# Performance work log

Measured on AMD Instinct MI355X. Metric: run time of the kernel, lower is better.

## Reference

```python
import jax, jax.numpy as jnp
import numpy as np

BETA_MIN, BETA_MAX = 0.01, 0.995
EPS_DELTA, EPS_RMS = 1e-6, 1e-5


def _rmsnorm(x, w):
    ms = jnp.mean(x * x, axis=-1, keepdims=True)
    return x * jax.lax.rsqrt(ms + EPS_RMS) * w


def _delta_scan(q, k, v, beta, mask, bb1, bb2):
    # q, k, v: [B, S, D]; beta, mask: [B, S, 1]; bb1, bb2: scalars
    phi_q = jax.nn.elu(q) + 1.0
    phi_k = jax.nn.elu(k) + 1.0
    b1_base = jnp.clip(jax.nn.sigmoid(bb1), BETA_MIN, BETA_MAX)
    b2_base = jnp.clip(jax.nn.sigmoid(bb2), BETA_MIN, BETA_MAX)
    B, S, D = q.shape

    def step(carry, inp):
        H1, H2, Z1, Z2 = carry
        qt, kt, vt, bt, mt = inp  # qt/kt/vt: [B,D], bt/mt: [B,1]
        bin_t = jnp.clip(bt, BETA_MIN, BETA_MAX)
        b1 = jnp.clip(b1_base * bin_t, BETA_MIN, BETA_MAX)  # [B,1]
        b2 = jnp.clip(b2_base * bin_t, BETA_MIN, BETA_MAX)
        kv = jnp.einsum('bd,be->bde', kt, vt) * mt[:, :, None]  # [B,D,D]
        H1 = H1 * b1[:, :, None] + kv
        H2 = H2 * b2[:, :, None] + kv
        km = kt * mt
        Z1 = Z1 * b1 + km
        Z2 = Z2 * b2 + km
        num = jnp.einsum('bd,bde->be', qt, H1 + H2)
        den = jnp.maximum(jnp.sum(qt * (Z1 + Z2), axis=-1, keepdims=True), EPS_DELTA)
        return (H1, H2, Z1, Z2), num / den * mt

    init = (jnp.zeros((B, D, D), q.dtype), jnp.zeros((B, D, D), q.dtype),
            jnp.zeros((B, D), q.dtype), jnp.zeros((B, D), q.dtype))
    xs = tuple(a.swapaxes(0, 1) for a in (phi_q, phi_k, v, beta, mask))
    _, outs = jax.lax.scan(step, init, xs)
    return outs.swapaxes(0, 1)  # [B, S, D]


def setup_inputs() -> dict:
    key = jax.random.key(0)
    B, S, Dm, H = 4, 2048, 512, 8
    ks = jax.random.split(key, 8)
    scale = float(1.0 / np.sqrt(Dm))
    return {
        'x': jax.random.normal(ks[0], (B, S, Dm), jnp.float32),
        'mask': jnp.ones((B, S), jnp.float32),
        'Wq': jax.random.normal(ks[1], (Dm, Dm), jnp.float32) * scale,
        'Wk': jax.random.normal(ks[2], (Dm, Dm), jnp.float32) * scale,
        'Wv': jax.random.normal(ks[3], (Dm, Dm), jnp.float32) * scale,
        'Wb': jax.random.normal(ks[4], (H, Dm), jnp.float32) * scale,
        'bb': jnp.full((H,), 1.5, jnp.float32),
        'Wo': jax.random.normal(ks[5], (Dm, Dm), jnp.float32) * scale,
        'bo': jnp.zeros((Dm,), jnp.float32),
        'ln_w': jnp.ones((Dm,), jnp.float32),
        'recency': jnp.zeros((H,), jnp.float32),
        'base_beta_1': jnp.asarray(2.0, jnp.float32),
        'base_beta_2': jnp.asarray(3.0, jnp.float32),
    }


def reference(x, mask, Wq, Wk, Wv, Wb, bb, Wo, bo, ln_w, recency,
              base_beta_1, base_beta_2):
    B, S, Dm = x.shape
    H = recency.shape[0]
    d = Dm // H
    h = _rmsnorm(x, ln_w)
    q = h @ Wq.T
    k = h @ Wk.T
    v = h @ Wv.T
    # input-conditioned gate with per-head recency bias  -> [B, S, H]
    beta = jax.nn.sigmoid(h @ Wb.T + bb + recency)

    def to_heads(t):  # [B,S,Dm] -> [B*H, S, d]
        return t.reshape(B, S, H, d).transpose(0, 2, 1, 3).reshape(B * H, S, d)

    qh, kh, vh = to_heads(q), to_heads(k), to_heads(v)
    betah = beta.transpose(0, 2, 1).reshape(B * H, S, 1)
    maskh = jnp.broadcast_to(mask[:, None, :, None], (B, H, S, 1)).reshape(B * H, S, 1)
    o = _delta_scan(qh, kh, vh, betah, maskh, base_beta_1, base_beta_2)
    o = o.reshape(B, H, S, d).transpose(0, 2, 1, 3).reshape(B, S, Dm)
    return x + (o @ Wo.T + bo)
```

## Files before the change

### kernel.cpp

```cpp
#include <hip/hip_runtime.h>
#include <stdint.h>

typedef unsigned short u16;
typedef short bf16x8 __attribute__((ext_vector_type(8)));
typedef unsigned short u16x8 __attribute__((ext_vector_type(8)));
typedef unsigned short u16x4 __attribute__((ext_vector_type(4)));
typedef float f32x4 __attribute__((ext_vector_type(4)));

#define S_ 2048
#define DM 512
#define DH 64
#define CL 64
#define NCH 32

#define SW(r, sc) ((r) * 72 + ((sc) ^ (((r) & 7) << 3)))

__device__ __forceinline__ float b2f(u16 u) { return __uint_as_float(((unsigned)u) << 16); }
__device__ __forceinline__ u16 f2b(float f) {
    unsigned v = __float_as_uint(f);
    unsigned r = v + 0x7fffu + ((v >> 16) & 1u);
    return (u16)(r >> 16);
}
__device__ __forceinline__ float phi_elu(float x) { return x > 0.f ? x + 1.f : __expf(x); }
__device__ __forceinline__ float clip01(float v) { return fminf(fmaxf(v, 0.01f), 0.995f); }

__device__ __forceinline__ void gload16(const u16* g, u16* l) {
    __builtin_amdgcn_global_load_lds((const __attribute__((address_space(1))) void*)g,
                                     (__attribute__((address_space(3))) void*)l, 16, 0, 0);
}

__global__ __launch_bounds__(256) void k_rb(const float* __restrict__ x, const float* __restrict__ lnw,
                                            const float* __restrict__ Wb, const float* __restrict__ bb,
                                            const float* __restrict__ rec, const float* __restrict__ bb1p,
                                            const float* __restrict__ bb2p, u16* __restrict__ h,
                                            float* __restrict__ lb1, float* __restrict__ lb2) {
    int wave = threadIdx.x >> 6, lane = threadIdx.x & 63;
    int row = blockIdx.x * 4 + wave;
    const float* xr = x + (size_t)row * DM + lane * 8;
    float4 v0 = *(const float4*)xr;
    float4 v1 = *(const float4*)(xr + 4);
    float ss = v0.x * v0.x + v0.y * v0.y + v0.z * v0.z + v0.w * v0.w +
               v1.x * v1.x + v1.y * v1.y + v1.z * v1.z + v1.w * v1.w;
    #pragma unroll
    for (int off = 32; off; off >>= 1) ss += __shfl_xor(ss, off, 64);
    float sc = rsqrtf(ss * (1.f / DM) + 1e-5f);
    const float* wr_ = lnw + lane * 8;
    float4 w0 = *(const float4*)wr_;
    float4 w1 = *(const float4*)(wr_ + 4);
    float hv[8];
    hv[0] = v0.x * sc * w0.x; hv[1] = v0.y * sc * w0.y;
    hv[2] = v0.z * sc * w0.z; hv[3] = v0.w * sc * w0.w;
    hv[4] = v1.x * sc * w1.x; hv[5] = v1.y * sc * w1.y;
    hv[6] = v1.z * sc * w1.z; hv[7] = v1.w * sc * w1.w;
    u16x8 o;
    #pragma unroll
    for (int j = 0; j < 8; j++) o[j] = f2b(hv[j]);
    *(u16x8*)(h + (size_t)row * DM + lane * 8) = o;
    float acc[8];
    #pragma unroll
    for (int hd = 0; hd < 8; hd++) {
        const float* wp = Wb + hd * DM + lane * 8;
        float4 a0 = *(const float4*)wp;
        float4 a1 = *(const float4*)(wp + 4);
        acc[hd] = hv[0] * a0.x + hv[1] * a0.y + hv[2] * a0.z + hv[3] * a0.w +
                  hv[4] * a1.x + hv[5] * a1.y + hv[6] * a1.z + hv[7] * a1.w;
    }
    #pragma unroll
    for (int hd = 0; hd < 8; hd++) {
        #pragma unroll
        for (int off = 32; off; off >>= 1) acc[hd] += __shfl_xor(acc[hd], off, 64);
    }
    if (lane == 0) {
        float b1b = clip01(1.f / (1.f + __expf(-bb1p[0])));
        float b2b = clip01(1.f / (1.f + __expf(-bb2p[0])));
        int b = row >> 11, s = row & 2047;
        #pragma unroll
        for (int hd = 0; hd < 8; hd++) {
            float logit = acc[hd] + bb[hd] + rec[hd];
            float beta = 1.f / (1.f + __expf(-logit));
            float bin = clip01(beta);
            float b1 = clip01(b1b * bin);
            float b2 = clip01(b2b * bin);
            size_t o2 = (size_t)((b << 3) + hd) * S_ + s;
            lb1[o2] = log2f(b1);
            lb2[o2] = log2f(b2);
        }
    }
}

__global__ __launch_bounds__(256) void k_convw(const float* __restrict__ Wq, const float* __restrict__ Wk,
                                               const float* __restrict__ Wv, const float* __restrict__ Wo,
                                               u16* __restrict__ wcat, u16* __restrict__ wo) {
    int idx = blockIdx.x * 256 + threadIdx.x;
    int e0 = idx << 2;
    if (e0 < 1536 * 512) {
        int r = e0 >> 9, ccol = e0 & 511;
        const float* src = (r < 512) ? (Wq + (size_t)r * 512)
                         : (r < 1024) ? (Wk + (size_t)(r - 512) * 512)
                                      : (Wv + (size_t)(r - 1024) * 512);
        float4 v = *(const float4*)(src + ccol);
        u16x4 o = {f2b(v.x), f2b(v.y), f2b(v.z), f2b(v.w)};
        *(u16x4*)(wcat + e0) = o;
    } else {
        int e = e0 - 1536 * 512;
        float4 v = *(const float4*)(Wo + e);
        u16x4 o = {f2b(v.x), f2b(v.y), f2b(v.z), f2b(v.w)};
        *(u16x4*)(wo + e) = o;
    }
}

template<int MODE>
__global__ __launch_bounds__(256) void k_gemm(const u16* __restrict__ A, const u16* __restrict__ Bw, int K,
                                              const float* __restrict__ mask, u16* __restrict__ qh,
                                              u16* __restrict__ kh, u16* __restrict__ vh,
                                              const float* __restrict__ xres, const float* __restrict__ bo,
                                              float* __restrict__ outp) {
    __shared__ u16 As[128 * 32];
    __shared__ u16 Bs[128 * 32];
    int tid = threadIdx.x;
    int lane = tid & 63, w = tid >> 6;
    int wr = w >> 1, wc = w & 1;
    int m0 = blockIdx.x * 128, n0 = blockIdx.y * 128;
    f32x4 acc[4][4] = {};
    int srow = w * 32 + (lane >> 2);
    int skel = (lane & 3) << 3;
    const u16* gA0 = A + (size_t)(m0 + srow) * K + skel;
    const u16* gA1 = gA0 + (size_t)16 * K;
    const u16* gB0 = Bw + (size_t)(n0 + srow) * K + skel;
    const u16* gB1 = gB0 + (size_t)16 * K;
    u16* lA0 = &As[(w * 32) * 32];
    u16* lA1 = &As[(w * 32 + 16) * 32];
    u16* lB0 = &Bs[(w * 32) * 32];
    u16* lB1 = &Bs[(w * 32 + 16) * 32];
    int l15 = lane & 15, kh8 = (lane >> 4) << 3;
    for (int k0 = 0; k0 < K; k0 += 32) {
        if (k0) __syncthreads();
        gload16(gA0 + k0, lA0);
        gload16(gA1 + k0, lA1);
        gload16(gB0 + k0, lB0);
        gload16(gB1 + k0, lB1);
        __syncthreads();
        bf16x8 af[4], bfr[4];
        #pragma unroll
        for (int m = 0; m < 4; m++) af[m] = *(const bf16x8*)&As[(wr * 64 + m * 16 + l15) * 32 + kh8];
        #pragma unroll
        for (int n = 0; n < 4; n++) bfr[n] = *(const bf16x8*)&Bs[(wc * 64 + n * 16 + l15) * 32 + kh8];
        #pragma unroll
        for (int m = 0; m < 4; m++)
            #pragma unroll
            for (int n = 0; n < 4; n++)
                acc[m][n] = __builtin_amdgcn_mfma_f32_16x16x32_bf16(af[m], bfr[n], acc[m][n], 0, 0, 0);
    }
    #pragma unroll
    for (int m = 0; m < 4; m++) {
        int rbase = m0 + wr * 64 + m * 16 + ((lane >> 4) << 2);
        #pragma unroll
        for (int n = 0; n < 4; n++) {
            int col = n0 + wc * 64 + n * 16 + l15;
            #pragma unroll
            for (int r = 0; r < 4; r++) {
                int row = rbase + r;
                float v = acc[m][n][r];
                if constexpr (MODE == 0) {
                    int mat = col >> 9, f = col & 511, hh = f >> 6, j = f & 63;
                    int b = row >> 11, s = row & 2047;
                    size_t di = ((size_t)((b << 3) + hh) * S_ + s) * DH + j;
                    if (mat == 0) qh[di] = f2b(phi_elu(v));
                    else if (mat == 1) kh[di] = f2b(phi_elu(v) * mask[(b << 11) + s]);
                    else vh[di] = f2b(v);
                } else {
                    size_t oi = (size_t)row * DM + col;
                    outp[oi] = v + xres[oi] + bo[col];
                }
            }
        }
    }
}

__global__ __launch_bounds__(256) void k_pass1(const u16* __restrict__ kh, const u16* __restrict__ vh,
                                               const float* __restrict__ lb1, const float* __restrict__ lb2,
                                               u16* __restrict__ S1b, u16* __restrict__ S2b,
                                               float* __restrict__ z1, float* __restrict__ z2,
                                               float* __restrict__ P1, float* __restrict__ P2) {
    __shared__ u16 Kw1[64 * 72];
    __shared__ u16 Kw2[64 * 72];
    __shared__ u16 Vt[64 * 72];
    __shared__ float Ls1[64], Ls2[64];
    int tid = threadIdx.x;
    int bh = blockIdx.x >> 5, c = blockIdx.x & 31;
    int wave = tid >> 6, lane = tid & 63;
    size_t base = ((size_t)bh * S_ + c * CL) * DH;
    if (wave == 0) {
        float v = lb1[(size_t)bh * S_ + c * CL + lane];
        #pragma unroll
        for (int d = 1; d < 64; d <<= 1) { float o = __shfl_up(v, d, 64); if (lane >= d) v += o; }
        Ls1[lane] = v;
    } else if (wave == 1) {
        float v = lb2[(size_t)bh * S_ + c * CL + lane];
        #pragma unroll
        for (int d = 1; d < 64; d <<= 1) { float o = __shfl_up(v, d, 64); if (lane >= d) v += o; }
        Ls2[lane] = v;
    }
    int ss = tid & 63, i0 = (tid >> 6) << 4;
    const u16* kr = kh + base + (size_t)ss * DH + i0;
    u16x8 kk0 = *(const u16x8*)kr;
    u16x8 kk1 = *(const u16x8*)(kr + 8);
    {
        const u16* vr = vh + base + (size_t)ss * DH + i0;
        u16x8 vv0 = *(const u16x8*)vr;
        u16x8 vv1 = *(const u16x8*)(vr + 8);
        #pragma unroll
        for (int j = 0; j < 8; j++) {
            Vt[SW(i0 + j, ss)] = vv0[j];
            Vt[SW(i0 + 8 + j, ss)] = vv1[j];
        }
    }
    __syncthreads();
    float w1 = exp2f(Ls1[63] - Ls1[ss]);
    float w2 = exp2f(Ls2[63] - Ls2[ss]);
    #pragma unroll
    for (int j = 0; j < 8; j++) {
        float k0 = b2f(kk0[j]), k1 = b2f(kk1[j]);
        Kw1[SW(i0 + j, ss)] = f2b(w1 * k0);
        Kw2[SW(i0 + j, ss)] = f2b(w2 * k0);
        Kw1[SW(i0 + 8 + j, ss)] = f2b(w1 * k1);
        Kw2[SW(i0 + 8 + j, ss)] = f2b(w2 * k1);
    }
    if (tid == 0) { P1[blockIdx.x] = exp2f(Ls1[63]); P2[blockIdx.x] = exp2f(Ls2[63]); }
    __syncthreads();
    int l15 = lane & 15, kh8 = (lane >> 4) << 3;
    int j0 = wave << 4;
    bf16x8 vf0 = *(const bf16x8*)&Vt[SW(j0 + l15, kh8)];
    bf16x8 vf1 = *(const bf16x8*)&Vt[SW(j0 + l15, 32 + kh8)];
    f32x4 a1[4], a2[4];
    #pragma unroll
    for (int it = 0; it < 4; it++) { a1[it] = (f32x4){0,0,0,0}; a2[it] = (f32x4){0,0,0,0}; }
    #pragma unroll
    for (int it = 0; it < 4; it++) {
        int ir = (it << 4) + l15;
        bf16x8 b0 = *(const bf16x8*)&Kw1[SW(ir, kh8)];
        bf16x8 b1 = *(const bf16x8*)&Kw1[SW(ir, 32 + kh8)];
        a1[it] = __builtin_amdgcn_mfma_f32_16x16x32_bf16(vf0, b0, a1[it], 0, 0, 0);
        a1[it] = __builtin_amdgcn_mfma_f32_16x16x32_bf16(vf1, b1, a1[it], 0, 0, 0);
        bf16x8 c0 = *(const bf16x8*)&Kw2[SW(ir, kh8)];
        bf16x8 c1 = *(const bf16x8*)&Kw2[SW(ir, 32 + kh8)];
        a2[it] = __builtin_amdgcn_mfma_f32_16x16x32_bf16(vf0, c0, a2[it], 0, 0, 0);
        a2[it] = __builtin_amdgcn_mfma_f32_16x16x32_bf16(vf1, c1, a2[it], 0, 0, 0);
    }
    {
        int iz = tid >> 2, sg = tid & 3;
        u16x8 x0 = *(const u16x8*)&Kw1[SW(iz, sg << 4)];
        u16x8 x1 = *(const u16x8*)&Kw1[SW(iz, (sg << 4) + 8)];
        u16x8 y0 = *(const u16x8*)&Kw2[SW(iz, sg << 4)];
        u16x8 y1 = *(const u16x8*)&Kw2[SW(iz, (sg << 4) + 8)];
        float z1v = 0.f, z2v = 0.f;
        #pragma unroll
        for (int j = 0; j < 8; j++) {
            z1v += b2f(x0[j]) + b2f(x1[j]);
            z2v += b2f(y0[j]) + b2f(y1[j]);
        }
        z1v += __shfl_xor(z1v, 1, 64); z1v += __shfl_xor(z1v, 2, 64);
        z2v += __shfl_xor(z2v, 1, 64); z2v += __shfl_xor(z2v, 2, 64);
        if (sg == 0) {
            z1[(size_t)blockIdx.x * 64 + iz] = z1v;
            z2[(size_t)blockIdx.x * 64 + iz] = z2v;
        }
    }
    int jr0 = j0 + ((lane >> 4) << 2);
    size_t so = (size_t)blockIdx.x * 4096;
    #pragma unroll
    for (int it = 0; it < 4; it++) {
        int ii = (it << 4) + l15;
        #pragma unroll
        for (int r = 0; r < 4; r++) {
            S1b[so + (size_t)(jr0 + r) * 64 + ii] = f2b(a1[it][r]);
            S2b[so + (size_t)(jr0 + r) * 64 + ii] = f2b(a2[it][r]);
        }
    }
}

__global__ __launch_bounds__(256) void k_pass2(u16* __restrict__ S1b, u16* __restrict__ S2b,
                                               float* __restrict__ z1, float* __restrict__ z2,
                                               const float* __restrict__ P1, const float* __restrict__ P2) {
    int bh = blockIdx.x >> 1, part = blockIdx.x & 1;
    int e0 = (part * 256 + threadIdx.x) * 8;
    float c1[8] = {}, c2[8] = {};
    for (int c = 0; c < NCH; c++) {
        int bc = bh * NCH + c;
        size_t idx = (size_t)bc * 4096 + e0;
        u16x8 s1 = *(const u16x8*)&S1b[idx];
        u16x8 s2 = *(const u16x8*)&S2b[idx];
        float p1 = P1[bc], p2 = P2[bc];
        u16x8 o1, o2;
        #pragma unroll
        for (int j = 0; j < 8; j++) {
            o1[j] = f2b(c1[j]); c1[j] = c1[j] * p1 + b2f(s1[j]);
            o2[j] = f2b(c2[j]); c2[j] = c2[j] * p2 + b2f(s2[j]);
        }
        *(u16x8*)&S1b[idx] = o1;
        *(u16x8*)&S2b[idx] = o2;
    }
    if (part == 0 && threadIdx.x < 64) {
        float y1 = 0.f, y2 = 0.f;
        for (int c = 0; c < NCH; c++) {
            int bc = bh * NCH + c;
            size_t zi = (size_t)bc * 64 + threadIdx.x;
            float p1 = P1[bc], p2 = P2[bc];
            float t1 = z1[zi]; z1[zi] = y1; y1 = y1 * p1 + t1;
            float t2 = z2[zi]; z2[zi] = y2; y2 = y2 * p2 + t2;
        }
    }
}

__global__ __launch_bounds__(256) void k_pass3(const u16* __restrict__ qh, const u16* __restrict__ kh,
                                               const u16* __restrict__ vh, const float* __restrict__ lb1,
                                               const float* __restrict__ lb2, const u16* __restrict__ S1b,
                                               const u16* __restrict__ S2b, const float* __restrict__ z1,
                                               const float* __restrict__ z2, const float* __restrict__ mask,
                                               u16* __restrict__ obf) {
    __shared__ u16 Vt[64 * 72];
    __shared__ u16 AWs[64 * 72];
    __shared__ float Ls1[64], Ls2[64], dens[64], qZ1[64], qZ2[64];
    int tid = threadIdx.x;
    int bh = blockIdx.x >> 5, c = blockIdx.x & 31;
    int wave = tid >> 6, lane = tid & 63;
    size_t base = ((size_t)bh * S_ + c * CL) * DH;
    if (wave == 0) {
        float v = lb1[(size_t)bh * S_ + c * CL + lane];
        #pragma unroll
        for (int d = 1; d < 64; d <<= 1) { float o = __shfl_up(v, d, 64); if (lane >= d) v += o; }
        Ls1[lane] = v;
    } else if (wave == 1) {
        float v = lb2[(size_t)bh * S_ + c * CL + lane];
        #pragma unroll
        for (int d = 1; d < 64; d <<= 1) { float o = __shfl_up(v, d, 64); if (lane >= d) v += o; }
        Ls2[lane] = v;
    }
    {
        int ss = tid & 63, i0 = (tid >> 6) << 4;
        const u16* vr = vh + base + (size_t)ss * DH + i0;
        u16x8 vv0 = *(const u16x8*)vr;
        u16x8 vv1 = *(const u16x8*)(vr + 8);
        #pragma unroll
        for (int j = 0; j < 8; j++) {
            Vt[SW(i0 + j, ss)] = vv0[j];
            Vt[SW(i0 + 8 + j, ss)] = vv1[j];
        }
    }
    {
        int t = tid >> 2, g = tid & 3;
        const u16* qp = qh + base + (size_t)t * DH + (g << 4);
        u16x8 q0 = *(const u16x8*)qp;
        u16x8 q1 = *(const u16x8*)(qp + 8);
        const float* z1p = z1 + (size_t)blockIdx.x * 64 + (g << 4);
        const float* z2p = z2 + (size_t)blockIdx.x * 64 + (g << 4);
        float az1 = 0.f, az2 = 0.f;
        #pragma unroll
        for (int m = 0; m < 8; m++) {
            float qv0 = b2f(q0[m]), qv1 = b2f(q1[m]);
            az1 += qv0 * z1p[m] + qv1 * z1p[m + 8];
            az2 += qv0 * z2p[m] + qv1 * z2p[m + 8];
        }
        az1 += __shfl_xor(az1, 1, 64); az1 += __shfl_xor(az1, 2, 64);
        az2 += __shfl_xor(az2, 1, 64); az2 += __shfl_xor(az2, 2, 64);
        if (g == 0) { qZ1[t] = az1; qZ2[t] = az2; }
    }
    int l15 = lane & 15, kh8 = (lane >> 4) << 3;
    int t0 = wave << 4;
    const u16* qb = qh + base + (size_t)(t0 + l15) * DH;
    bf16x8 qf0 = *(const bf16x8*)(qb + kh8);
    bf16x8 qf1 = *(const bf16x8*)(qb + 32 + kh8);
    f32x4 accA[4];
    #pragma unroll
    for (int st = 0; st < 4; st++) accA[st] = (f32x4){0, 0, 0, 0};
    #pragma unroll
    for (int st = 0; st < 4; st++) {
        const u16* kb = kh + base + (size_t)((st << 4) + l15) * DH;
        bf16x8 kf0 = *(const bf16x8*)(kb + kh8);
        bf16x8 kf1 = *(const bf16x8*)(kb + 32 + kh8);
        accA[st] = __builtin_amdgcn_mfma_f32_16x16x32_bf16(qf0, kf0, accA[st], 0, 0, 0);
        accA[st] = __builtin_amdgcn_mfma_f32_16x16x32_bf16(qf1, kf1, accA[st], 0, 0, 0);
    }
    __syncthreads();
    int trow = t0 + ((lane >> 4) << 2);
    float l1t[4], l2t[4];
    #pragma unroll
    for (int r = 0; r < 4; r++) { l1t[r] = Ls1[trow + r]; l2t[r] = Ls2[trow + r]; }
    float rs[4] = {0.f, 0.f, 0.f, 0.f};
    #pragma unroll
    for (int st = 0; st < 4; st++) {
        int s = (st << 4) + l15;
        float s1 = Ls1[s], s2 = Ls2[s];
        #pragma unroll
        for (int r = 0; r < 4; r++) {
            float w = 0.f;
            if (s <= trow + r) w = exp2f(l1t[r] - s1) + exp2f(l2t[r] - s2);
            u16 awb = f2b(accA[st][r] * w);
            AWs[SW(trow + r, s)] = awb;
            rs[r] += b2f(awb);
        }
    }
    #pragma unroll
    for (int off = 1; off < 16; off <<= 1) {
        #pragma unroll
        for (int r = 0; r < 4; r++) rs[r] += __shfl_xor(rs[r], off, 64);
    }
    if (l15 == 0) {
        #pragma unroll
        for (int r = 0; r < 4; r++) dens[trow + r] = rs[r];
    }
    __syncthreads();
    bf16x8 awf0 = *(const bf16x8*)&AWs[SW(t0 + l15, kh8)];
    bf16x8 awf1 = *(const bf16x8*)&AWs[SW(t0 + l15, 32 + kh8)];
    const u16* h1g = S1b + (size_t)blockIdx.x * 4096;
    const u16* h2g = S2b + (size_t)blockIdx.x * 4096;
    f32x4 accO[4], accC1[4], accC2[4];
    #pragma unroll
    for (int jt = 0; jt < 4; jt++) {
        accO[jt] = (f32x4){0, 0, 0, 0};
        accC1[jt] = (f32x4){0, 0, 0, 0};
        accC2[jt] = (f32x4){0, 0, 0, 0};
    }
    #pragma unroll
    for (int jt = 0; jt < 4; jt++) {
        int jr = (jt << 4) + l15;
        bf16x8 v0 = *(const bf16x8*)&Vt[SW(jr, kh8)];
        bf16x8 v1 = *(const bf16x8*)&Vt[SW(jr, 32 + kh8)];
        accO[jt] = __builtin_amdgcn_mfma_f32_16x16x32_bf16(awf0, v0, accO[jt], 0, 0, 0);
        accO[jt] = __builtin_amdgcn_mfma_f32_16x16x32_bf16(awf1, v1, accO[jt], 0, 0, 0);
        bf16x8 h10 = *(const bf16x8*)(h1g + (size_t)jr * 64 + kh8);
        bf16x8 h11 = *(const bf16x8*)(h1g + (size_t)jr * 64 + 32 + kh8);
        accC1[jt] = __builtin_amdgcn_mfma_f32_16x16x32_bf16(qf0, h10, accC1[jt], 0, 0, 0);
        accC1[jt] = __builtin_amdgcn_mfma_f32_16x16x32_bf16(qf1, h11, accC1[jt], 0, 0, 0);
        bf16x8 h20 = *(const bf16x8*)(h2g + (size_t)jr * 64 + kh8);
        bf16x8 h21 = *(const bf16x8*)(h2g + (size_t)jr * 64 + 32 + kh8);
        accC2[jt] = __builtin_amdgcn_mfma_f32_16x16x32_bf16(qf0, h20, accC2[jt], 0, 0, 0);
        accC2[jt] = __builtin_amdgcn_mfma_f32_16x16x32_bf16(qf1, h21, accC2[jt], 0, 0, 0);
    }
    int b = bh >> 3, hh = bh & 7;
    #pragma unroll
    for (int r = 0; r < 4; r++) {
        int t = trow + r;
        float e1 = exp2f(l1t[r]), e2 = exp2f(l2t[r]);
        float den = dens[t] + e1 * qZ1[t] + e2 * qZ2[t];
        den = fmaxf(den, 1e-6f);
        int sg = (c << 6) + t;
        float mv = mask[(size_t)b * S_ + sg];
        float inv = mv / den;
        u16* op = obf + ((size_t)b * S_ + sg) * DM + hh * DH;
        #pragma unroll
        for (int jt = 0; jt < 4; jt++) {
            float numv = accO[jt][r] + e1 * accC1[jt][r] + e2 * accC2[jt][r];
            op[(jt << 4) + l15] = f2b(numv * inv);
        }
    }
}

extern "C" void kernel_launch(void* const* d_in, const int* in_sizes, int n_in,
                              void* d_out, int out_size, void* d_ws, size_t ws_size,
                              hipStream_t stream) {
    const float* x    = (const float*)d_in[0];
    const float* mask = (const float*)d_in[1];
    const float* Wq   = (const float*)d_in[2];
    const float* Wk   = (const float*)d_in[3];
    const float* Wv   = (const float*)d_in[4];
    const float* Wb   = (const float*)d_in[5];
    const float* bb   = (const float*)d_in[6];
    const float* Wo   = (const float*)d_in[7];
    const float* bo   = (const float*)d_in[8];
    const float* lnw  = (const float*)d_in[9];
    const float* rec  = (const float*)d_in[10];
    const float* bb1  = (const float*)d_in[11];
    const float* bb2  = (const float*)d_in[12];
    float* out = (float*)d_out;

    char* w = (char*)d_ws;
    u16* h    = (u16*)w;  w += (size_t)8192 * 512 * 2;
    u16* wcat = (u16*)w;  w += (size_t)1536 * 512 * 2;
    u16* wo   = (u16*)w;  w += (size_t)512 * 512 * 2;
    u16* qh   = (u16*)w;  w += (size_t)8192 * 512 * 2;
    u16* kh   = (u16*)w;  w += (size_t)8192 * 512 * 2;
    u16* vh   = (u16*)w;  w += (size_t)8192 * 512 * 2;
    float* lb1 = (float*)w; w += (size_t)32 * 2048 * 4;
    float* lb2 = (float*)w; w += (size_t)32 * 2048 * 4;
    u16* S1b  = (u16*)w;  w += (size_t)1024 * 4096 * 2;
    u16* S2b  = (u16*)w;  w += (size_t)1024 * 4096 * 2;
    float* z1  = (float*)w; w += (size_t)1024 * 64 * 4;
    float* z2  = (float*)w; w += (size_t)1024 * 64 * 4;
    float* P1  = (float*)w; w += 4096;
    float* P2  = (float*)w; w += 4096;
    u16* obf   = (u16*)w;   w += (size_t)8192 * 512 * 2;

    k_rb<<<2048, 256, 0, stream>>>(x, lnw, Wb, bb, rec, bb1, bb2, h, lb1, lb2);
    k_convw<<<1024, 256, 0, stream>>>(Wq, Wk, Wv, Wo, wcat, wo);
    k_gemm<0><<<dim3(64, 12), 256, 0, stream>>>(h, wcat, 512, mask, qh, kh, vh, nullptr, nullptr, nullptr);
    k_pass1<<<1024, 256, 0, stream>>>(kh, vh, lb1, lb2, S1b, S2b, z1, z2, P1, P2);
    k_pass2<<<64, 256, 0, stream>>>(S1b, S2b, z1, z2, P1, P2);
    k_pass3<<<1024, 256, 0, stream>>>(qh, kh, vh, lb1, lb2, S1b, S2b, z1, z2, mask, obf);
    k_gemm<1><<<dim3(64, 4), 256, 0, stream>>>(obf, wo, 512, nullptr, nullptr, nullptr, nullptr, x, bo, out);
}
```

Before: 118.9 us.

## Spread pass2 chunk-prefix scan over more blocks and XCD-remap GEMM tiles

The inter-chunk state prefix pass now runs on 512 blocks, one state element per thread, plus 8 blocks for the normaliser scan, instead of 64 blocks doing 8 elements each. The aim is to fill the GPU during this serial-over-chunks pass. The GEMM kernels also remap workgroup IDs so that consecutive logical tiles land on the same XCD, which should improve L2 reuse of shared A/B rows. The trade-off is that each pass2 thread now does scalar 2-byte loads and stores instead of 16-byte vector accesses.

```diff
diff --git a/kernel.cpp b/kernel.cpp
--- a/kernel.cpp
+++ b/kernel.cpp
@@ -109,7 +109,7 @@
     }
 }
 
-template<int MODE>
+template<int MODE, int NT>
 __global__ __launch_bounds__(256) void k_gemm(const u16* __restrict__ A, const u16* __restrict__ Bw, int K,
                                               const float* __restrict__ mask, u16* __restrict__ qh,
                                               u16* __restrict__ kh, u16* __restrict__ vh,
@@ -120,7 +120,12 @@
     int tid = threadIdx.x;
     int lane = tid & 63, w = tid >> 6;
     int wr = w >> 1, wc = w & 1;
-    int m0 = blockIdx.x * 128, n0 = blockIdx.y * 128;
+    int hwid = blockIdx.y * gridDim.x + blockIdx.x;
+    int nwg = gridDim.x * NT;
+    int q8 = nwg >> 3;
+    int logical = (hwid & 7) * q8 + (hwid >> 3);
+    int mTile = logical / NT, nTile = logical % NT;
+    int m0 = mTile * 128, n0 = nTile * 128;
     f32x4 acc[4][4] = {};
     int srow = w * 32 + (lane >> 2);
     int skel = (lane & 3) << 3;
@@ -282,29 +287,27 @@
 __global__ __launch_bounds__(256) void k_pass2(u16* __restrict__ S1b, u16* __restrict__ S2b,
                                                float* __restrict__ z1, float* __restrict__ z2,
                                                const float* __restrict__ P1, const float* __restrict__ P2) {
-    int bh = blockIdx.x >> 1, part = blockIdx.x & 1;
-    int e0 = (part * 256 + threadIdx.x) * 8;
-    float c1[8] = {}, c2[8] = {};
-    for (int c = 0; c < NCH; c++) {
-        int bc = bh * NCH + c;
-        size_t idx = (size_t)bc * 4096 + e0;
-        u16x8 s1 = *(const u16x8*)&S1b[idx];
-        u16x8 s2 = *(const u16x8*)&S2b[idx];
-        float p1 = P1[bc], p2 = P2[bc];
-        u16x8 o1, o2;
-        #pragma unroll
-        for (int j = 0; j < 8; j++) {
-            o1[j] = f2b(c1[j]); c1[j] = c1[j] * p1 + b2f(s1[j]);
-            o2[j] = f2b(c2[j]); c2[j] = c2[j] * p2 + b2f(s2[j]);
-        }
-        *(u16x8*)&S1b[idx] = o1;
-        *(u16x8*)&S2b[idx] = o2;
-    }
-    if (part == 0 && threadIdx.x < 64) {
-        float y1 = 0.f, y2 = 0.f;
+    int blk = blockIdx.x;
+    if (blk < 512) {
+        int bh = blk >> 4;
+        int e = ((blk & 15) << 8) + threadIdx.x;
+        float c1 = 0.f, c2 = 0.f;
+        #pragma unroll 4
         for (int c = 0; c < NCH; c++) {
             int bc = bh * NCH + c;
-            size_t zi = (size_t)bc * 64 + threadIdx.x;
+            size_t idx = (size_t)bc * 4096 + e;
+            float p1 = P1[bc], p2 = P2[bc];
+            float t1 = b2f(S1b[idx]); S1b[idx] = f2b(c1); c1 = c1 * p1 + t1;
+            float t2 = b2f(S2b[idx]); S2b[idx] = f2b(c2); c2 = c2 * p2 + t2;
+        }
+    } else {
+        int bh = ((blk - 512) << 2) + (threadIdx.x >> 6);
+        int e = threadIdx.x & 63;
+        float y1 = 0.f, y2 = 0.f;
+        #pragma unroll 4
+        for (int c = 0; c < NCH; c++) {
+            int bc = bh * NCH + c;
+            size_t zi = (size_t)bc * 64 + e;
             float p1 = P1[bc], p2 = P2[bc];
             float t1 = z1[zi]; z1[zi] = y1; y1 = y1 * p1 + t1;
             float t2 = z2[zi]; z2[zi] = y2; y2 = y2 * p2 + t2;
@@ -493,9 +496,9 @@
 
     k_rb<<<2048, 256, 0, stream>>>(x, lnw, Wb, bb, rec, bb1, bb2, h, lb1, lb2);
     k_convw<<<1024, 256, 0, stream>>>(Wq, Wk, Wv, Wo, wcat, wo);
-    k_gemm<0><<<dim3(64, 12), 256, 0, stream>>>(h, wcat, 512, mask, qh, kh, vh, nullptr, nullptr, nullptr);
+    k_gemm<0, 12><<<dim3(64, 12), 256, 0, stream>>>(h, wcat, 512, mask, qh, kh, vh, nullptr, nullptr, nullptr);
     k_pass1<<<1024, 256, 0, stream>>>(kh, vh, lb1, lb2, S1b, S2b, z1, z2, P1, P2);
-    k_pass2<<<64, 256, 0, stream>>>(S1b, S2b, z1, z2, P1, P2);
+    k_pass2<<<520, 256, 0, stream>>>(S1b, S2b, z1, z2, P1, P2);
     k_pass3<<<1024, 256, 0, stream>>>(qh, kh, vh, lb1, lb2, S1b, S2b, z1, z2, mask, obf);
-    k_gemm<1><<<dim3(64, 4), 256, 0, stream>>>(obf, wo, 512, nullptr, nullptr, nullptr, nullptr, x, bo, out);
-}
+    k_gemm<1, 4><<<dim3(64, 4), 256, 0, stream>>>(obf, wo, 512, nullptr, nullptr, nullptr, nullptr, x, bo, out);
+}
```

New measurement: 112.3 us. -5.5%, faster.
